# Kernel optimization log

Hardware: AMD Instinct MI355X
Metric: run time of the kernel (lower is better)

Reference implementation:

```python
import jax, jax.numpy as jnp
import numpy as np
import math

B, T, C = 2, 2048, 1024
NH = 16
HD = C // NH

def setup_inputs() -> dict:
    key = jax.random.key(0)
    ks = jax.random.split(key, 3)
    scale = 0.02
    return {
        "x": jax.random.normal(ks[0], (B, T, C), dtype=jnp.float32),
        "Wqkv": jax.random.normal(ks[1], (C, 3 * C), dtype=jnp.float32) * scale,
        "bqkv": jnp.zeros((3 * C,), dtype=jnp.float32),
        "Wproj": jax.random.normal(ks[2], (C, C), dtype=jnp.float32) * scale,
        "bproj": jnp.zeros((C,), dtype=jnp.float32),
    }

def reference(x, Wqkv, bqkv, Wproj, bproj):
    b, t, c = x.shape
    qkv = x @ Wqkv + bqkv                      # (B,T,3C)
    qkv = qkv.reshape(b, t, 3, NH, HD)
    q = jnp.transpose(qkv[:, :, 0], (0, 2, 1, 3))  # (B,H,T,D)
    k = jnp.transpose(qkv[:, :, 1], (0, 2, 1, 3))
    v = jnp.transpose(qkv[:, :, 2], (0, 2, 1, 3))
    att = jnp.einsum('bhqd,bhkd->bhqk', q, k) / math.sqrt(HD)
    causal = jnp.tril(jnp.ones((t, t), dtype=bool))
    att = jnp.where(causal[None, None], att, jnp.float32(-jnp.inf))
    att = jax.nn.softmax(att, axis=-1)
    y = jnp.einsum('bhqk,bhkd->bhqd', att, v)  # (B,H,T,D)
    y = jnp.transpose(y, (0, 2, 1, 3)).reshape(b, t, c)
    return y @ Wproj + bproj
```

## Files before the change

kernel.cpp:

```cpp
#include <hip/hip_runtime.h>


typedef __attribute__((ext_vector_type(8))) short short8;
typedef __attribute__((ext_vector_type(4))) short short4v;
typedef __attribute__((ext_vector_type(4))) float f32x4;
typedef __attribute__((ext_vector_type(2))) unsigned int u32x2;
struct ushort4_t { unsigned short x, y, z, w; };

#define MFMA16(a, b, c) __builtin_amdgcn_mfma_f32_16x16x32_bf16((a), (b), (c), 0, 0, 0)
#define MFMA16K16(a, b, c) __builtin_amdgcn_mfma_f32_16x16x16bf16_1k((a), (b), (c), 0, 0, 0)

__device__ __forceinline__ unsigned short f2bf(float f) {
  unsigned u = __builtin_bit_cast(unsigned, f);
  u += 0x7fffu + ((u >> 16) & 1u);
  return (unsigned short)(u >> 16);
}

__device__ __forceinline__ unsigned short f2bf_fast(float f) {
  return (unsigned short)((__builtin_bit_cast(unsigned, f) + 0x8000u) >> 16);
}

#if __has_builtin(__builtin_amdgcn_cvt_pk_bf16_f32)
typedef __attribute__((ext_vector_type(2))) __bf16 bf16x2;
__device__ __forceinline__ short4v pack_bf16x4(float a, float b, float c, float d) {
  bf16x2 lo = __builtin_amdgcn_cvt_pk_bf16_f32(a, b);
  bf16x2 hi = __builtin_amdgcn_cvt_pk_bf16_f32(c, d);
  u32x2 t;
  t[0] = __builtin_bit_cast(unsigned, lo);
  t[1] = __builtin_bit_cast(unsigned, hi);
  return __builtin_bit_cast(short4v, t);
}
#else
__device__ __forceinline__ short4v pack_bf16x4(float a, float b, float c, float d) {
  short4v r;
  r[0] = (short)f2bf_fast(a); r[1] = (short)f2bf_fast(b);
  r[2] = (short)f2bf_fast(c); r[3] = (short)f2bf_fast(d);
  return r;
}
#endif

__device__ __forceinline__ void gl2lds16(const void* g, void* l) {
  __builtin_amdgcn_global_load_lds(
      (__attribute__((address_space(1))) void*)g,
      (__attribute__((address_space(3))) void*)l,
      16, 0, 0);
}

__global__ __launch_bounds__(256)
void prep(const float* __restrict__ x, unsigned short* __restrict__ xb,
          const float* __restrict__ Wqkv, unsigned short* __restrict__ wqkvT,
          const float* __restrict__ Wproj, unsigned short* __restrict__ wprojT) {
  __shared__ float tile[64][65];
  const int bx = blockIdx.x, tid = threadIdx.x;
  if (bx < 4096) {
    const int i = (bx * 256 + tid) * 4;
    float4 f = *(const float4*)(x + i);
    unsigned long long r = (unsigned long long)f2bf(f.x)
        | ((unsigned long long)f2bf(f.y) << 16)
        | ((unsigned long long)f2bf(f.z) << 32)
        | ((unsigned long long)f2bf(f.w) << 48);
    *(unsigned long long*)(xb + i) = r;
    return;
  }
  const float* W;
  unsigned short* WT;
  int n0, k0, N;
  if (bx < 4864) {
    const int idx = bx - 4096;
    W = Wqkv; WT = wqkvT; N = 3072;
    n0 = (idx % 48) * 64; k0 = (idx / 48) * 64;
  } else {
    const int idx = bx - 4864;
    W = Wproj; WT = wprojT; N = 1024;
    n0 = (idx % 16) * 64; k0 = (idx / 16) * 64;
  }
  const int K = 1024;
  const int c = tid & 63, rbase = tid >> 6;
#pragma unroll
  for (int i = 0; i < 16; ++i) {
    int r = i * 4 + rbase;
    tile[r][c] = W[(size_t)(k0 + r) * N + n0 + c];
  }
  __syncthreads();
#pragma unroll
  for (int i = 0; i < 16; ++i) {
    int r = i * 4 + rbase;
    WT[(size_t)(n0 + r) * K + k0 + c] = f2bf(tile[c][r]);
  }
}

template <int EPI, int MT>
__global__ __launch_bounds__(256)
void gemm_bt(const unsigned short* __restrict__ A,
             const unsigned short* __restrict__ BT,
             const float* __restrict__ bias,
             float* __restrict__ outF,
             unsigned short* __restrict__ q_out,
             unsigned short* __restrict__ k_out,
             unsigned short* __restrict__ vT_out,
             int Ndim, int Kdim) {
  constexpr int IF = MT / 32;
  constexpr int RA = MT / 32;
  __shared__ __align__(16) unsigned short As[MT * 64];
  __shared__ __align__(16) unsigned short Bs[128 * 64];
  const int tid = threadIdx.x;
  const int wave = tid >> 6, lane = tid & 63;
  const int quad = lane >> 4, lr = lane & 15;
  const int wm = wave >> 1, wn = wave & 1;
  const int m0 = blockIdx.y * MT, n0 = blockIdx.x * 128;

  const int r_l = tid >> 3;
  const int cg = (tid & 7) ^ (r_l & 7);
  const unsigned short* gA = A + (size_t)(m0 + r_l) * Kdim + cg * 8;
  const unsigned short* gB = BT + (size_t)(n0 + r_l) * Kdim + cg * 8;
  const size_t rstep = (size_t)32 * Kdim;

  f32x4 acc[IF][4] = {};
  for (int k0 = 0; k0 < Kdim; k0 += 64) {
#pragma unroll
    for (int rd = 0; rd < RA; ++rd)
      gl2lds16(gA + k0 + rd * rstep, As + rd * 2048 + wave * 512);
#pragma unroll
    for (int rd = 0; rd < 4; ++rd)
      gl2lds16(gB + k0 + rd * rstep, Bs + rd * 2048 + wave * 512);
    __syncthreads();
#pragma unroll
    for (int s = 0; s < 2; ++s) {
      const int sw = ((s * 4 + quad) ^ (lr & 7)) * 8;
      short8 a[IF], b[4];
#pragma unroll
      for (int i = 0; i < IF; ++i)
        a[i] = *(const short8*)(As + (wm * (MT / 2) + i * 16 + lr) * 64 + sw);
#pragma unroll
      for (int j = 0; j < 4; ++j)
        b[j] = *(const short8*)(Bs + (wn * 64 + j * 16 + lr) * 64 + sw);
#pragma unroll
      for (int i = 0; i < IF; ++i)
#pragma unroll
        for (int j = 0; j < 4; ++j)
          acc[i][j] = MFMA16(a[i], b[j], acc[i][j]);
    }
    __syncthreads();
  }

  const int row_t = wm * (MT / 2) + quad * 4;
  const int col_t = wn * 64 + lr;
  if (EPI == 0) {
    const int sec = n0 >> 10;
    const float scl = (sec == 0) ? 0.18033688f : 1.0f;
#pragma unroll
    for (int j = 0; j < 4; ++j) {
      const int n = n0 + col_t + j * 16;
      const float bi = bias[n];
      const int nn = n & 1023, h = nn >> 6, d = nn & 63;
#pragma unroll
      for (int i = 0; i < IF; ++i) {
        const int m_base = m0 + row_t + i * 16;
        const int bb = m_base >> 11, t0 = m_base & 2047;
        const int bh = bb * 16 + h;
        if (sec == 2) {
          ushort4_t pk;
          pk.x = f2bf(acc[i][j][0] + bi);
          pk.y = f2bf(acc[i][j][1] + bi);
          pk.z = f2bf(acc[i][j][2] + bi);
          pk.w = f2bf(acc[i][j][3] + bi);
          *(ushort4_t*)(vT_out + ((size_t)bh * 64 + d) * 2048 + t0) = pk;
        } else {
          unsigned short* dst = (sec == 0 ? q_out : k_out) + (size_t)bh * 131072 + t0 * 64 + d;
#pragma unroll
          for (int r = 0; r < 4; ++r)
            dst[r * 64] = f2bf((acc[i][j][r] + bi) * scl);
        }
      }
    }
  } else {
#pragma unroll
    for (int i = 0; i < IF; ++i)
#pragma unroll
      for (int r = 0; r < 4; ++r) {
        const int m = m0 + row_t + i * 16 + r;
#pragma unroll
        for (int j = 0; j < 4; ++j) {
          const int n = n0 + col_t + j * 16;
          outF[(size_t)m * Ndim + n] = acc[i][j][r] + bias[n];
        }
      }
  }
}

__global__ __launch_bounds__(256, 3)
void attn(const unsigned short* __restrict__ qbuf,
          const unsigned short* __restrict__ kbuf,
          const unsigned short* __restrict__ vT,
          unsigned short* __restrict__ yb) {
  __shared__ __align__(16) unsigned short Ks[3][4096];
  __shared__ __align__(16) unsigned short Vs[3][4096];
  const int tid = threadIdx.x, wave = tid >> 6, lane = tid & 63;
  const int quad = lane >> 4, lr = lane & 15;
  const int bh = blockIdx.x;
  const int qt = 31 - (int)blockIdx.y;
  const int qrow0 = qt * 64;

  const unsigned short* qp0 = qbuf + (size_t)bh * 131072;
  const unsigned short* kp0 = kbuf + (size_t)bh * 131072;
  const unsigned short* vp0 = vT   + (size_t)bh * 131072;

  short8 aq[2];
  {
    const unsigned short* qp =
        qp0 + (size_t)(qrow0 + wave * 16 + lr) * 64 + quad * 8;
    aq[0] = *(const short8*)qp;
    aq[1] = *(const short8*)(qp + 32);
  }

  short4v ones4;
#pragma unroll
  for (int i = 0; i < 4; ++i) ones4[i] = (short)0x3F80;

  const int sr = tid >> 3;
  const int scg = (tid & 7) ^ (sr & 7);
  int kbase[2];
#pragma unroll
  for (int h = 0; h < 2; ++h)
    kbase[h] = lr * 64 + (((quad + 4 * h) ^ (lr & 7)) << 3);
  int vbase[4];
#pragma unroll
  for (int kb = 0; kb < 4; ++kb)
    vbase[kb] = lr * 64 + (((2 * kb + (quad >> 1)) ^ (lr & 7)) << 3) + (quad & 1) * 4;

  f32x4 o[4] = {};
  f32x4 lacc = {};

  auto stage = [&](int buf, int kt) {
    const unsigned short* kg = kp0 + (size_t)(kt * 64 + sr) * 64 + scg * 8;
    const unsigned short* vg = vp0 + (size_t)sr * 2048 + kt * 64 + scg * 8;
    gl2lds16(kg,             &Ks[buf][wave * 512]);
    gl2lds16(kg + 32 * 64,   &Ks[buf][2048 + wave * 512]);
    gl2lds16(vg,             &Vs[buf][wave * 512]);
    gl2lds16(vg + 32 * 2048, &Vs[buf][2048 + wave * 512]);
  };

  const int dlast = qt;
  stage(0, 0);
  if (dlast >= 1) stage(1, 1);
  int buf = 0;
  for (int kt = 0; kt <= dlast; ++kt) {
    if (kt < dlast) __builtin_amdgcn_s_waitcnt(0x0F74);
    else            __builtin_amdgcn_s_waitcnt(0x0F70);
    __builtin_amdgcn_s_barrier();
    if (kt + 2 <= dlast) {
      int nb = buf + 2; if (nb >= 3) nb -= 3;
      stage(nb, kt + 2);
    }
    const unsigned short* Kb = Ks[buf];
    const unsigned short* Vb = Vs[buf];
    short8 bk[4][2];
#pragma unroll
    for (int jt = 0; jt < 4; ++jt) {
      bk[jt][0] = *(const short8*)(Kb + jt * 1024 + kbase[0]);
      bk[jt][1] = *(const short8*)(Kb + jt * 1024 + kbase[1]);
    }
    f32x4 s[4] = {};
    __builtin_amdgcn_s_setprio(1);
#pragma unroll
    for (int jt = 0; jt < 4; ++jt) {
      s[jt] = MFMA16(bk[jt][0], aq[0], s[jt]);
      s[jt] = MFMA16(bk[jt][1], aq[1], s[jt]);
    }
    __builtin_amdgcn_s_setprio(0);
    short4v pa[4];
    if (kt == dlast) {
      const int qloc = wave * 16 + lr;
#pragma unroll
      for (int jt = 0; jt < 4; ++jt) {
        float p[4];
#pragma unroll
        for (int r = 0; r < 4; ++r) {
          p[r] = __builtin_amdgcn_exp2f(s[jt][r]);
          if (jt * 16 + quad * 4 + r > qloc) p[r] = 0.f;
        }
        pa[jt] = pack_bf16x4(p[0], p[1], p[2], p[3]);
      }
    } else {
#pragma unroll
      for (int jt = 0; jt < 4; ++jt) {
        float p[4];
#pragma unroll
        for (int r = 0; r < 4; ++r) p[r] = __builtin_amdgcn_exp2f(s[jt][r]);
        pa[jt] = pack_bf16x4(p[0], p[1], p[2], p[3]);
      }
    }
    __builtin_amdgcn_s_setprio(1);
#pragma unroll
    for (int kb = 0; kb < 4; ++kb)
      lacc = MFMA16K16(ones4, pa[kb], lacc);
#pragma unroll
    for (int kb = 0; kb < 4; ++kb)
#pragma unroll
      for (int jd = 0; jd < 4; ++jd) {
        const short4v bv = *(const short4v*)(Vb + jd * 1024 + vbase[kb]);
        o[jd] = MFMA16K16(pa[kb], bv, o[jd]);
      }
    __builtin_amdgcn_s_setprio(0);
    buf += 1; if (buf >= 3) buf -= 3;
  }

  const int b = bh >> 4, h = bh & 15;
  float inv[4];
#pragma unroll
  for (int r = 0; r < 4; ++r)
    inv[r] = __builtin_amdgcn_rcpf(__shfl(lacc[0], quad * 4 + r));
#pragma unroll
  for (int jd = 0; jd < 4; ++jd)
#pragma unroll
    for (int r = 0; r < 4; ++r) {
      const int t = qrow0 + wave * 16 + quad * 4 + r;
      yb[((size_t)b * 2048 + t) * 1024 + h * 64 + jd * 16 + lr] =
          f2bf(o[jd][r] * inv[r]);
    }
}

extern "C" void kernel_launch(void* const* d_in, const int* in_sizes, int n_in,
                              void* d_out, int out_size, void* d_ws, size_t ws_size,
                              hipStream_t stream) {
  const float* x     = (const float*)d_in[0];
  const float* Wqkv  = (const float*)d_in[1];
  const float* bqkv  = (const float*)d_in[2];
  const float* Wproj = (const float*)d_in[3];
  const float* bproj = (const float*)d_in[4];
  float* out = (float*)d_out;

  char* ws = (char*)d_ws;
  unsigned short* xb     = (unsigned short*)(ws);
  unsigned short* wqkvT  = (unsigned short*)(ws + 8388608);
  unsigned short* wprojT = (unsigned short*)(ws + 14680064);
  unsigned short* qbuf   = (unsigned short*)(ws + 16777216);
  unsigned short* kbuf   = (unsigned short*)(ws + 25165824);
  unsigned short* vTbuf  = (unsigned short*)(ws + 33554432);
  unsigned short* ybuf   = (unsigned short*)(ws + 41943040);

  prep<<<5120, 256, 0, stream>>>(x, xb, Wqkv, wqkvT, Wproj, wprojT);
  gemm_bt<0, 128><<<dim3(24, 32), 256, 0, stream>>>(xb, wqkvT, bqkv, nullptr,
                                                    qbuf, kbuf, vTbuf, 3072, 1024);
  attn<<<dim3(32, 32), 256, 0, stream>>>(qbuf, kbuf, vTbuf, ybuf);
  gemm_bt<1, 64><<<dim3(8, 64), 256, 0, stream>>>(ybuf, wprojT, bproj, out,
                                                  nullptr, nullptr, nullptr, 1024, 1024);
}
```

Before: 177.3 us.

## Double-buffer attention K/V with higher occupancy and interleaved causal tile order

The attention kernel drops from triple to double buffering of K/V tiles in LDS, prefetching one tile ahead, and raises launch bounds from 3 to 4 blocks per CU. The smaller LDS footprint is meant to let more blocks stay resident to hide latency. Query tiles are also reordered so heavy and light causal tiles alternate across blockIdx.y, for better load balance. The GEMM main loop is moved into a helper and the V-store packing is tidied. The risk is less prefetch depth, which exposes load latency per tile, and tighter register limits.

```diff
diff --git a/kernel.cpp b/kernel.cpp
--- a/kernel.cpp
+++ b/kernel.cpp
@@ -5,7 +5,6 @@
 typedef __attribute__((ext_vector_type(4))) short short4v;
 typedef __attribute__((ext_vector_type(4))) float f32x4;
 typedef __attribute__((ext_vector_type(2))) unsigned int u32x2;
-struct ushort4_t { unsigned short x, y, z, w; };
 
 #define MFMA16(a, b, c) __builtin_amdgcn_mfma_f32_16x16x32_bf16((a), (b), (c), 0, 0, 0)
 #define MFMA16K16(a, b, c) __builtin_amdgcn_mfma_f32_16x16x16bf16_1k((a), (b), (c), 0, 0, 0)
@@ -38,6 +37,13 @@
   return r;
 }
 #endif
+
+__device__ __forceinline__ short4v pack_rne4(float a, float b, float c, float d) {
+  short4v r;
+  r[0] = (short)f2bf(a); r[1] = (short)f2bf(b);
+  r[2] = (short)f2bf(c); r[3] = (short)f2bf(d);
+  return r;
+}
 
 __device__ __forceinline__ void gl2lds16(const void* g, void* l) {
   __builtin_amdgcn_global_load_lds(
@@ -89,6 +95,44 @@
   }
 }
 
+template <int MT>
+__device__ __forceinline__ void gemm_core(
+    const unsigned short* __restrict__ gA,
+    const unsigned short* __restrict__ gB,
+    unsigned short* As, unsigned short* Bs,
+    int Kdim, int wave, int quad, int lr, int wm, int wn,
+    f32x4 (&acc)[MT / 32][4]) {
+  constexpr int IF = MT / 32;
+  constexpr int RA = MT / 32;
+  const size_t rstep = (size_t)32 * Kdim;
+  for (int k0 = 0; k0 < Kdim; k0 += 64) {
+#pragma unroll
+    for (int rd = 0; rd < RA; ++rd)
+      gl2lds16(gA + k0 + rd * rstep, As + rd * 2048 + wave * 512);
+#pragma unroll
+    for (int rd = 0; rd < 4; ++rd)
+      gl2lds16(gB + k0 + rd * rstep, Bs + rd * 2048 + wave * 512);
+    __syncthreads();
+#pragma unroll
+    for (int s = 0; s < 2; ++s) {
+      const int sw = ((s * 4 + quad) ^ (lr & 7)) * 8;
+      short8 a[IF], b[4];
+#pragma unroll
+      for (int i = 0; i < IF; ++i)
+        a[i] = *(const short8*)(As + (wm * (MT / 2) + i * 16 + lr) * 64 + sw);
+#pragma unroll
+      for (int j = 0; j < 4; ++j)
+        b[j] = *(const short8*)(Bs + (wn * 64 + j * 16 + lr) * 64 + sw);
+#pragma unroll
+      for (int i = 0; i < IF; ++i)
+#pragma unroll
+        for (int j = 0; j < 4; ++j)
+          acc[i][j] = MFMA16(a[i], b[j], acc[i][j]);
+    }
+    __syncthreads();
+  }
+}
+
 template <int EPI, int MT>
 __global__ __launch_bounds__(256)
 void gemm_bt(const unsigned short* __restrict__ A,
@@ -100,7 +144,6 @@
              unsigned short* __restrict__ vT_out,
              int Ndim, int Kdim) {
   constexpr int IF = MT / 32;
-  constexpr int RA = MT / 32;
   __shared__ __align__(16) unsigned short As[MT * 64];
   __shared__ __align__(16) unsigned short Bs[128 * 64];
   const int tid = threadIdx.x;
@@ -113,39 +156,13 @@
   const int cg = (tid & 7) ^ (r_l & 7);
   const unsigned short* gA = A + (size_t)(m0 + r_l) * Kdim + cg * 8;
   const unsigned short* gB = BT + (size_t)(n0 + r_l) * Kdim + cg * 8;
-  const size_t rstep = (size_t)32 * Kdim;
 
   f32x4 acc[IF][4] = {};
-  for (int k0 = 0; k0 < Kdim; k0 += 64) {
-#pragma unroll
-    for (int rd = 0; rd < RA; ++rd)
-      gl2lds16(gA + k0 + rd * rstep, As + rd * 2048 + wave * 512);
-#pragma unroll
-    for (int rd = 0; rd < 4; ++rd)
-      gl2lds16(gB + k0 + rd * rstep, Bs + rd * 2048 + wave * 512);
-    __syncthreads();
-#pragma unroll
-    for (int s = 0; s < 2; ++s) {
-      const int sw = ((s * 4 + quad) ^ (lr & 7)) * 8;
-      short8 a[IF], b[4];
-#pragma unroll
-      for (int i = 0; i < IF; ++i)
-        a[i] = *(const short8*)(As + (wm * (MT / 2) + i * 16 + lr) * 64 + sw);
-#pragma unroll
-      for (int j = 0; j < 4; ++j)
-        b[j] = *(const short8*)(Bs + (wn * 64 + j * 16 + lr) * 64 + sw);
-#pragma unroll
-      for (int i = 0; i < IF; ++i)
-#pragma unroll
-        for (int j = 0; j < 4; ++j)
-          acc[i][j] = MFMA16(a[i], b[j], acc[i][j]);
-    }
-    __syncthreads();
-  }
+  gemm_core<MT>(gA, gB, As, Bs, Kdim, wave, quad, lr, wm, wn, acc);
 
   const int row_t = wm * (MT / 2) + quad * 4;
   const int col_t = wn * 64 + lr;
-  if (EPI == 0) {
+  if constexpr (EPI == 0) {
     const int sec = n0 >> 10;
     const float scl = (sec == 0) ? 0.18033688f : 1.0f;
 #pragma unroll
@@ -159,12 +176,9 @@
         const int bb = m_base >> 11, t0 = m_base & 2047;
         const int bh = bb * 16 + h;
         if (sec == 2) {
-          ushort4_t pk;
-          pk.x = f2bf(acc[i][j][0] + bi);
-          pk.y = f2bf(acc[i][j][1] + bi);
-          pk.z = f2bf(acc[i][j][2] + bi);
-          pk.w = f2bf(acc[i][j][3] + bi);
-          *(ushort4_t*)(vT_out + ((size_t)bh * 64 + d) * 2048 + t0) = pk;
+          short4v pk = pack_rne4(acc[i][j][0] + bi, acc[i][j][1] + bi,
+                                 acc[i][j][2] + bi, acc[i][j][3] + bi);
+          *(short4v*)(vT_out + ((size_t)bh * 64 + d) * 2048 + t0) = pk;
         } else {
           unsigned short* dst = (sec == 0 ? q_out : k_out) + (size_t)bh * 131072 + t0 * 64 + d;
 #pragma unroll
@@ -188,17 +202,22 @@
   }
 }
 
-__global__ __launch_bounds__(256, 3)
+__global__ __launch_bounds__(256, 4)
 void attn(const unsigned short* __restrict__ qbuf,
           const unsigned short* __restrict__ kbuf,
           const unsigned short* __restrict__ vT,
           unsigned short* __restrict__ yb) {
-  __shared__ __align__(16) unsigned short Ks[3][4096];
-  __shared__ __align__(16) unsigned short Vs[3][4096];
+  __shared__ __align__(16) unsigned short Ks[2][4096];
+  __shared__ __align__(16) unsigned short Vs[2][4096];
   const int tid = threadIdx.x, wave = tid >> 6, lane = tid & 63;
   const int quad = lane >> 4, lr = lane & 15;
   const int bh = blockIdx.x;
-  const int qt = 31 - (int)blockIdx.y;
+  const int by = blockIdx.y;
+  int qt;
+  if (by < 8)       qt = 31 - by;
+  else if (by < 16) qt = by - 8;
+  else if (by < 24) qt = 39 - by;
+  else              qt = by - 16;
   const int qrow0 = qt * 64;
 
   const unsigned short* qp0 = qbuf + (size_t)bh * 131072;
@@ -242,18 +261,13 @@
 
   const int dlast = qt;
   stage(0, 0);
-  if (dlast >= 1) stage(1, 1);
-  int buf = 0;
+  int cur = 0;
   for (int kt = 0; kt <= dlast; ++kt) {
-    if (kt < dlast) __builtin_amdgcn_s_waitcnt(0x0F74);
-    else            __builtin_amdgcn_s_waitcnt(0x0F70);
+    __builtin_amdgcn_s_waitcnt(0x0F70);
     __builtin_amdgcn_s_barrier();
-    if (kt + 2 <= dlast) {
-      int nb = buf + 2; if (nb >= 3) nb -= 3;
-      stage(nb, kt + 2);
-    }
-    const unsigned short* Kb = Ks[buf];
-    const unsigned short* Vb = Vs[buf];
+    if (kt + 1 <= dlast) stage(cur ^ 1, kt + 1);
+    const unsigned short* Kb = Ks[cur];
+    const unsigned short* Vb = Vs[cur];
     short8 bk[4][2];
 #pragma unroll
     for (int jt = 0; jt < 4; ++jt) {
@@ -302,7 +316,7 @@
         o[jd] = MFMA16K16(pa[kb], bv, o[jd]);
       }
     __builtin_amdgcn_s_setprio(0);
-    buf += 1; if (buf >= 3) buf -= 3;
+    cur ^= 1;
   }
 
   const int b = bh >> 4, h = bh & 15;
```

New measurement: 182.2 us. 2.7% more time.
